# Kernel tuning notes

Hardware: AMD Instinct MI355X
Metric: run time of the kernel (lower is better)

## Reference

```python
import jax, jax.numpy as jnp
import numpy as np

MARGIN = 0.1
LAMDA = 1.0


def setup_inputs() -> dict:
    key = jax.random.key(0)
    k1, k2, k3 = jax.random.split(key, 3)
    B, C, D = 256, 4096, 100
    return {
        "feat_pos": jax.random.normal(k1, (B, D), dtype=jnp.float32),
        "feat_neg": jax.random.normal(k2, (B, C, D), dtype=jnp.float32),
        "feat_lan": jax.random.normal(k3, (B, D), dtype=jnp.float32),
    }


def reference(feat_pos, feat_neg, feat_lan):
    # loss1: overall mean squared distance between pos and lang features
    loss1 = jnp.mean((feat_pos - feat_lan) ** 2)
    # loss2: hinge on per-(b,c) mean squared distance pos vs each neg clip
    # d2[b, c] = mean_d (pos[b, d] - neg[b, c, d])^2
    d2 = jnp.mean((feat_pos[:, None, :] - feat_neg) ** 2, axis=-1)  # (B, C)
    loss2 = jnp.mean(jax.nn.relu(MARGIN - d2))  # sum / (B*C)
    return loss1 + LAMDA * loss2
```

## Files before the change

kernel.cpp:

```cpp
#include <hip/hip_runtime.h>

#define MARGIN 0.1f
#define BB 256
#define CC 4096
#define DD 100
#define CBLK 256

__global__ __launch_bounds__(256) void loss1_kernel(const float* __restrict__ pos,
                                                    const float* __restrict__ lan,
                                                    float* __restrict__ out) {
    const int tid = threadIdx.x;
    const int N = BB * DD;
    float s = 0.f;
    for (int i = tid; i < N; i += 256) {
        float d = pos[i] - lan[i];
        s += d * d;
    }
    #pragma unroll
    for (int off = 32; off >= 1; off >>= 1)
        s += __shfl_xor(s, off, 64);
    __shared__ float ws[4];
    const int w = tid >> 6;
    if ((tid & 63) == 0) ws[w] = s;
    __syncthreads();
    if (tid == 0) {
        float t = ws[0] + ws[1] + ws[2] + ws[3];
        out[0] = t * (1.f / (float)N);
    }
}

__global__ __launch_bounds__(256) void loss2_kernel(const float* __restrict__ pos,
                                                    const float* __restrict__ neg,
                                                    float* __restrict__ out) {
    const int b    = blockIdx.x;
    const int c0   = blockIdx.y * CBLK;
    const int tid  = threadIdx.x;
    const int lane = tid & 63;
    const int w    = tid >> 6;

    __shared__ float pos_s[DD];
    if (tid < DD) pos_s[tid] = pos[b * DD + tid];
    __syncthreads();

    float p0 = 0.f, p1 = 0.f;
    if (lane < 50) {
        p0 = pos_s[2 * lane];
        p1 = pos_s[2 * lane + 1];
    }

    const float* negb = neg + (size_t)b * ((size_t)CC * DD);
    const int cw = c0 + (w << 6);
    float acc = 0.f;

    #pragma unroll 2
    for (int i = 0; i < 64; ++i) {
        const int c = cw + i;
        float v0 = 0.f, v1 = 0.f;
        if (lane < 50) {
            const float2 v = *(const float2*)(negb + (size_t)c * DD + 2 * lane);
            v0 = v.x; v1 = v.y;
        }
        const float d0 = p0 - v0;
        const float d1 = p1 - v1;
        float s = d0 * d0 + d1 * d1;
        #pragma unroll
        for (int off = 32; off >= 1; off >>= 1)
            s += __shfl_xor(s, off, 64);
        acc += fmaxf(MARGIN - s * (1.f / (float)DD), 0.f);
    }

    __shared__ float ws2[4];
    if (lane == 0) ws2[w] = acc;
    __syncthreads();
    if (tid == 0) {
        const float t = ws2[0] + ws2[1] + ws2[2] + ws2[3];
        atomicAdd(out, t * (1.f / ((float)BB * (float)CC)));
    }
}

extern "C" void kernel_launch(void* const* d_in, const int* in_sizes, int n_in,
                              void* d_out, int out_size, void* d_ws, size_t ws_size,
                              hipStream_t stream) {
    const float* pos = (const float*)d_in[0];
    const float* neg = (const float*)d_in[1];
    const float* lan = (const float*)d_in[2];
    float* out = (float*)d_out;

    loss1_kernel<<<1, 256, 0, stream>>>(pos, lan, out);
    loss2_kernel<<<dim3(BB, CC / CBLK), 256, 0, stream>>>(pos, neg, out);
}
```

Baseline: 628.2 us.

## Map one thread per negative row and fuse loss1 into the main kernel

Replaces the wave-per-row scheme, where 50 of 64 lanes load float2 and every row needs a six-step shuffle reduction, with one thread per (b,c) row. Each thread reads its own 400-byte row as 25 float4 loads and accumulates the squared distance in registers. The separate loss1 launch is folded into the first c-block of each batch row, and the output is zeroed with a memset before the kernel. In exchange, lanes in a wave now read addresses 400 bytes apart, so this relies on the L1/L2 caches to absorb the strided, uncoalesced access pattern.

New measurement: 573.8 us. -8.7%, faster.

```diff
diff --git a/kernel.cpp b/kernel.cpp
--- a/kernel.cpp
+++ b/kernel.cpp
@@ -4,78 +4,50 @@
 #define BB 256
 #define CC 4096
 #define DD 100
-#define CBLK 256
+#define TPB 256
 
-__global__ __launch_bounds__(256) void loss1_kernel(const float* __restrict__ pos,
-                                                    const float* __restrict__ lan,
-                                                    float* __restrict__ out) {
+__global__ __launch_bounds__(TPB) void amloss_kernel(const float* __restrict__ pos,
+                                                     const float* __restrict__ neg,
+                                                     const float* __restrict__ lan,
+                                                     float* __restrict__ out) {
     const int tid = threadIdx.x;
-    const int N = BB * DD;
-    float s = 0.f;
-    for (int i = tid; i < N; i += 256) {
-        float d = pos[i] - lan[i];
-        s += d * d;
-    }
-    #pragma unroll
-    for (int off = 32; off >= 1; off >>= 1)
-        s += __shfl_xor(s, off, 64);
-    __shared__ float ws[4];
-    const int w = tid >> 6;
-    if ((tid & 63) == 0) ws[w] = s;
-    __syncthreads();
-    if (tid == 0) {
-        float t = ws[0] + ws[1] + ws[2] + ws[3];
-        out[0] = t * (1.f / (float)N);
-    }
-}
+    const int b   = blockIdx.y;
+    const int c   = blockIdx.x * TPB + tid;
 
-__global__ __launch_bounds__(256) void loss2_kernel(const float* __restrict__ pos,
-                                                    const float* __restrict__ neg,
-                                                    float* __restrict__ out) {
-    const int b    = blockIdx.x;
-    const int c0   = blockIdx.y * CBLK;
-    const int tid  = threadIdx.x;
-    const int lane = tid & 63;
-    const int w    = tid >> 6;
-
-    __shared__ float pos_s[DD];
+    __shared__ __align__(16) float pos_s[DD];
     if (tid < DD) pos_s[tid] = pos[b * DD + tid];
     __syncthreads();
 
-    float p0 = 0.f, p1 = 0.f;
-    if (lane < 50) {
-        p0 = pos_s[2 * lane];
-        p1 = pos_s[2 * lane + 1];
+    const float4* __restrict__ row =
+        (const float4*)(neg + ((size_t)b * CC + (size_t)c) * DD);
+    const float4* __restrict__ pos4 = (const float4*)pos_s;
+
+    float s = 0.f;
+    #pragma unroll
+    for (int k = 0; k < DD / 4; ++k) {
+        const float4 v = row[k];
+        const float4 p = pos4[k];
+        const float d0 = p.x - v.x;
+        const float d1 = p.y - v.y;
+        const float d2 = p.z - v.z;
+        const float d3 = p.w - v.w;
+        s += d0 * d0 + d1 * d1 + d2 * d2 + d3 * d3;
+    }
+    float contrib = fmaxf(MARGIN - s * (1.f / (float)DD), 0.f)
+                  * (1.f / ((float)BB * (float)CC));
+
+    if (blockIdx.x == 0 && tid < DD) {
+        const float d = pos_s[tid] - lan[b * DD + tid];
+        contrib += d * d * (1.f / ((float)BB * (float)DD));
     }
 
-    const float* negb = neg + (size_t)b * ((size_t)CC * DD);
-    const int cw = c0 + (w << 6);
-    float acc = 0.f;
-
-    #pragma unroll 2
-    for (int i = 0; i < 64; ++i) {
-        const int c = cw + i;
-        float v0 = 0.f, v1 = 0.f;
-        if (lane < 50) {
-            const float2 v = *(const float2*)(negb + (size_t)c * DD + 2 * lane);
-            v0 = v.x; v1 = v.y;
-        }
-        const float d0 = p0 - v0;
-        const float d1 = p1 - v1;
-        float s = d0 * d0 + d1 * d1;
-        #pragma unroll
-        for (int off = 32; off >= 1; off >>= 1)
-            s += __shfl_xor(s, off, 64);
-        acc += fmaxf(MARGIN - s * (1.f / (float)DD), 0.f);
-    }
-
-    __shared__ float ws2[4];
-    if (lane == 0) ws2[w] = acc;
+    #pragma unroll
+    for (int off = 32; off >= 1; off >>= 1)
+        contrib += __shfl_xor(contrib, off, 64);
+    __shared__ float ws[4];
+    if ((tid & 63) == 0) ws[tid >> 6] = contrib;
     __syncthreads();
-    if (tid == 0) {
-        const float t = ws2[0] + ws2[1] + ws2[2] + ws2[3];
-        atomicAdd(out, t * (1.f / ((float)BB * (float)CC)));
-    }
+    if (tid == 0) atomicAdd(out, ws[0] + ws[1] + ws[2] + ws[3]);
 }
 
 extern "C" void kernel_launch(void* const* d_in, const int* in_sizes, int n_in,
@@ -86,6 +58,7 @@
     const float* lan = (const float*)d_in[2];
     float* out = (float*)d_out;
 
-    loss1_kernel<<<1, 256, 0, stream>>>(pos, lan, out);
-    loss2_kernel<<<dim3(BB, CC / CBLK), 256, 0, stream>>>(pos, neg, out);
+    hipMemsetAsync(out, 0, (size_t)out_size * sizeof(float), stream);
+
+    amloss_kernel<<<dim3(CC / TPB, BB), TPB, 0, stream>>>(pos, neg, lan, out);
 }
```
